# Kernel optimization log

Hardware: AMD Instinct MI355X
Metric: run time of the kernel (lower is better)

The kernel has to match this reference:

```python
import jax, jax.numpy as jnp
import numpy as np

M = 512          # n_clusters
D_PER = 32       # examples per cluster
FEAT = 1024      # embedding dim
ALPHA = 1.0
N_CLASSES = 128
EPS = 1e-8


def setup_inputs() -> dict:
    key = jax.random.key(0)
    k1, k2 = jax.random.split(key)
    N = M * D_PER
    inp = jax.random.normal(k1, (N, FEAT), dtype=jnp.float32)
    # class label per cluster, repeated d times so each contiguous chunk shares a class
    cluster_classes = jax.random.randint(k2, (M,), 0, N_CLASSES, dtype=jnp.int32)
    target = jnp.repeat(cluster_classes, D_PER)
    return {"input": inp, "target": target}


def reference(input, target):
    N, feat = input.shape
    m, d = M, D_PER
    # cluster assignment: sorted arange(m) repeated d times == repeat(arange(m), d)
    clusters = jnp.repeat(jnp.arange(m), d)                      # [N]
    cluster_classes = target[0 : m * d : d]                      # [m]

    # segment mean over contiguous equal-size chunks (== torch.chunk + mean + stack)
    means = input.reshape(m, d, feat).mean(axis=1)               # [m, feat]

    r2 = jnp.sum(input * input, axis=1, keepdims=True)           # [N,1]
    c2 = jnp.sum(means * means, axis=1)                          # [m]
    sample_costs = r2 + c2[None, :] - 2.0 * (input @ means.T)    # [N, m]

    # distance of each example to its own cluster mean
    intra = jnp.take_along_axis(sample_costs, clusters[:, None], axis=1)[:, 0]  # [N]

    variance = jnp.sum(intra) / float(N - 1)
    var_norm = -1.0 / (2.0 * variance ** 2)

    numerator = jnp.exp(var_norm * intra - ALPHA)                # [N]

    diff_class_mask = (target[:, None] != cluster_classes[None, :]).astype(input.dtype)  # [N,m]
    denominator = jnp.sum(diff_class_mask * jnp.exp(var_norm * sample_costs), axis=1)    # [N]

    losses = jax.nn.relu(-jnp.log(numerator / (denominator + EPS) + EPS))
    total_loss = jnp.mean(losses)

    pred = jnp.argmin(sample_costs, axis=1)                      # [N]
    acc = jnp.mean((pred == clusters).astype(jnp.float32))
    return total_loss, losses, pred, acc
```

## Files before the change

kernel.cpp:

```cpp
#include <hip/hip_runtime.h>
#include <math.h>

#define NCLUST 512
#define DPER 32
#define NFEAT 1024
#define NSAMP (NCLUST * DPER)
#define ALPHA_C 1.0f
#define EPS_C 1e-8f
#define MARGIN_C 0.25f

#define GBM 128
#define GBN 128
#define GBK 32
#define NCHUNK 8

typedef __attribute__((ext_vector_type(4))) float f32x4;
typedef __attribute__((ext_vector_type(8))) _Float16 f16x8;

__device__ __forceinline__ unsigned f2h(float f) {
  _Float16 h = (_Float16)f;
  return (unsigned)__builtin_bit_cast(ushort, h);
}

__device__ __forceinline__ void gload16(const ushort* g, ushort* l) {
  __builtin_amdgcn_global_load_lds(
      (const __attribute__((address_space(1))) unsigned int*)g,
      (__attribute__((address_space(3))) unsigned int*)l, 16, 0, 0);
}

__global__ __launch_bounds__(256) void k_pre(const float* __restrict__ inp,
                                             const int* __restrict__ target,
                                             float* __restrict__ means,
                                             ushort* __restrict__ Bf16,
                                             ushort* __restrict__ Af16,
                                             float* __restrict__ c2,
                                             float* __restrict__ r2g,
                                             float* __restrict__ intra,
                                             float* __restrict__ percl,
                                             int* __restrict__ ccls,
                                             int* __restrict__ wcount) {
  const int m = blockIdx.x;
  const int t = threadIdx.x;
  const int w = t >> 6, l = t & 63;
  __shared__ float ldsm[4][NFEAT];
  __shared__ float meanf[NFEAT];
  __shared__ float red4[4];
  __shared__ float redi[4];
  __shared__ float c2sh;

  const float* rowbase = inp + (size_t)m * DPER * NFEAT;
  ushort* arowbase = Af16 + (size_t)m * DPER * NFEAT;

  float4 macc0 = {0,0,0,0}, macc1 = {0,0,0,0}, macc2 = {0,0,0,0}, macc3 = {0,0,0,0};
  float r2keep[8];

  #pragma unroll 2
  for (int rr = 0; rr < 8; ++rr) {
    const int d = w * 8 + rr;
    const float* rp = rowbase + (size_t)d * NFEAT + l * 4;
    const float4 v0 = *(const float4*)(rp);
    const float4 v1 = *(const float4*)(rp + 256);
    const float4 v2 = *(const float4*)(rp + 512);
    const float4 v3 = *(const float4*)(rp + 768);
    ushort* ap = arowbase + (size_t)d * NFEAT + l * 4;
    uint2 h;
    h.x = f2h(v0.x) | (f2h(v0.y) << 16); h.y = f2h(v0.z) | (f2h(v0.w) << 16);
    *(uint2*)(ap) = h;
    h.x = f2h(v1.x) | (f2h(v1.y) << 16); h.y = f2h(v1.z) | (f2h(v1.w) << 16);
    *(uint2*)(ap + 256) = h;
    h.x = f2h(v2.x) | (f2h(v2.y) << 16); h.y = f2h(v2.z) | (f2h(v2.w) << 16);
    *(uint2*)(ap + 512) = h;
    h.x = f2h(v3.x) | (f2h(v3.y) << 16); h.y = f2h(v3.z) | (f2h(v3.w) << 16);
    *(uint2*)(ap + 768) = h;
    macc0.x += v0.x; macc0.y += v0.y; macc0.z += v0.z; macc0.w += v0.w;
    macc1.x += v1.x; macc1.y += v1.y; macc1.z += v1.z; macc1.w += v1.w;
    macc2.x += v2.x; macc2.y += v2.y; macc2.z += v2.z; macc2.w += v2.w;
    macc3.x += v3.x; macc3.y += v3.y; macc3.z += v3.z; macc3.w += v3.w;
    float p = v0.x*v0.x + v0.y*v0.y + v0.z*v0.z + v0.w*v0.w
            + v1.x*v1.x + v1.y*v1.y + v1.z*v1.z + v1.w*v1.w
            + v2.x*v2.x + v2.y*v2.y + v2.z*v2.z + v2.w*v2.w
            + v3.x*v3.x + v3.y*v3.y + v3.z*v3.z + v3.w*v3.w;
    #pragma unroll
    for (int off = 32; off; off >>= 1) p += __shfl_down(p, off);
    r2keep[rr] = p;
  }
  if (l == 0) {
    #pragma unroll
    for (int rr = 0; rr < 8; ++rr) r2g[m * DPER + w * 8 + rr] = r2keep[rr];
  }
  *(float4*)&ldsm[w][0 * 256 + l * 4] = macc0;
  *(float4*)&ldsm[w][1 * 256 + l * 4] = macc1;
  *(float4*)&ldsm[w][2 * 256 + l * 4] = macc2;
  *(float4*)&ldsm[w][3 * 256 + l * 4] = macc3;
  __syncthreads();
  float4 s0 = *(const float4*)&ldsm[0][t * 4];
  float4 s1 = *(const float4*)&ldsm[1][t * 4];
  float4 s2 = *(const float4*)&ldsm[2][t * 4];
  float4 s3 = *(const float4*)&ldsm[3][t * 4];
  const float inv = 1.0f / 32.0f;
  float4 mn;
  mn.x = (s0.x + s1.x + s2.x + s3.x) * inv;
  mn.y = (s0.y + s1.y + s2.y + s3.y) * inv;
  mn.z = (s0.z + s1.z + s2.z + s3.z) * inv;
  mn.w = (s0.w + s1.w + s2.w + s3.w) * inv;
  *(float4*)(means + (size_t)m * NFEAT + t * 4) = mn;
  uint2 bw;
  bw.x = f2h(mn.x) | (f2h(mn.y) << 16);
  bw.y = f2h(mn.z) | (f2h(mn.w) << 16);
  *(uint2*)&Bf16[(size_t)m * NFEAT + t * 4] = bw;
  *(float4*)&meanf[t * 4] = mn;
  float sq = mn.x * mn.x + mn.y * mn.y + mn.z * mn.z + mn.w * mn.w;
  #pragma unroll
  for (int off = 32; off; off >>= 1) sq += __shfl_down(sq, off);
  if (l == 0) red4[w] = sq;
  __syncthreads();
  if (t == 0) {
    const float cc = red4[0] + red4[1] + red4[2] + red4[3];
    c2sh = cc;
    c2[m] = cc;
    ccls[m] = target[m * DPER];
    if (m == 0) *wcount = 0;
  }
  __syncthreads();
  const float c2v = c2sh;
  float sintra = 0.f;
  #pragma unroll 2
  for (int rr = 0; rr < 8; ++rr) {
    const int d = w * 8 + rr;
    const float* rp = rowbase + (size_t)d * NFEAT + l * 4;
    const float4 v0 = *(const float4*)(rp);
    const float4 v1 = *(const float4*)(rp + 256);
    const float4 v2 = *(const float4*)(rp + 512);
    const float4 v3 = *(const float4*)(rp + 768);
    const float4 m0 = *(const float4*)&meanf[0 * 256 + l * 4];
    const float4 m1 = *(const float4*)&meanf[1 * 256 + l * 4];
    const float4 m2 = *(const float4*)&meanf[2 * 256 + l * 4];
    const float4 m3 = *(const float4*)&meanf[3 * 256 + l * 4];
    float p = v0.x*m0.x + v0.y*m0.y + v0.z*m0.z + v0.w*m0.w
            + v1.x*m1.x + v1.y*m1.y + v1.z*m1.z + v1.w*m1.w
            + v2.x*m2.x + v2.y*m2.y + v2.z*m2.z + v2.w*m2.w
            + v3.x*m3.x + v3.y*m3.y + v3.z*m3.z + v3.w*m3.w;
    #pragma unroll
    for (int off = 32; off; off >>= 1) p += __shfl_down(p, off);
    if (l == 0) {
      const float iv = r2keep[rr] + c2v - 2.0f * p;
      intra[m * DPER + d] = iv;
      sintra += iv;
    }
  }
  if (l == 0) redi[w] = sintra;
  __syncthreads();
  if (t == 0) percl[m] = redi[0] + redi[1] + redi[2] + redi[3];
}

__global__ __launch_bounds__(256) void k_var(const float* __restrict__ percl,
                                             float* __restrict__ vn) {
  const int t = threadIdx.x;
  float s = percl[t] + percl[t + 256];
  __shared__ float red[4];
  #pragma unroll
  for (int off = 32; off > 0; off >>= 1) s += __shfl_down(s, off);
  if ((t & 63) == 0) red[t >> 6] = s;
  __syncthreads();
  if (t == 0) {
    float tot = red[0] + red[1] + red[2] + red[3];
    float var = tot / (float)(NSAMP - 1);
    vn[0] = -1.0f / (2.0f * var * var);
  }
}

__global__ __launch_bounds__(256, 3) void k_gemm(
    const ushort* __restrict__ Af16, const ushort* __restrict__ Bf16,
    const float* __restrict__ c2, const float* __restrict__ r2,
    const float* __restrict__ vnp, const int* __restrict__ ccls,
    const int* __restrict__ target,
    float* __restrict__ den_p, float* __restrict__ minv_p,
    float* __restrict__ minv2_p, float* __restrict__ minc_p) {
  __shared__ ushort As[GBM * GBK];
  __shared__ ushort Bs[GBN * GBK];
  const int t = threadIdx.x;
  const int l = t & 63, w = t >> 6;
  const int wg = (blockIdx.x & 7) * 64 + (blockIdx.x >> 3);
  const int rowblk = wg >> 2, colblk = wg & 3;
  const int row0 = rowblk * GBM, c0 = colblk * GBN;
  const int wr = w >> 1, wc = w & 1;

  const int sR = l >> 2;
  const int sg = (l & 3) ^ (sR & 3);
  const ushort* srcA0 = Af16 + (size_t)(row0 + w * 32 + sR) * NFEAT + sg * 8;
  const ushort* srcA1 = srcA0 + 16 * NFEAT;
  const ushort* srcB0 = Bf16 + (size_t)(c0 + w * 32 + sR) * NFEAT + sg * 8;
  const ushort* srcB1 = srcB0 + 16 * NFEAT;
  ushort* ldsA0 = As + w * 32 * GBK;
  ushort* ldsA1 = ldsA0 + 16 * GBK;
  ushort* ldsB0 = Bs + w * 32 * GBK;
  ushort* ldsB1 = ldsB0 + 16 * GBK;

  const int fr = l & 15, fq = l >> 4;
  const int ch = ((fq ^ (fr & 3)) * 8);

  f32x4 acc[4][4];
  #pragma unroll
  for (int i = 0; i < 4; ++i)
    #pragma unroll
    for (int j = 0; j < 4; ++j) acc[i][j] = (f32x4){0.f, 0.f, 0.f, 0.f};

  for (int ks = 0; ks < NFEAT / GBK; ++ks) {
    __syncthreads();
    gload16(srcA0, ldsA0); gload16(srcA1, ldsA1);
    gload16(srcB0, ldsB0); gload16(srcB1, ldsB1);
    srcA0 += GBK; srcA1 += GBK; srcB0 += GBK; srcB1 += GBK;
    __syncthreads();
    f16x8 a[4], b[4];
    #pragma unroll
    for (int i = 0; i < 4; ++i)
      a[i] = *(const f16x8*)&As[(wr * 64 + i * 16 + fr) * GBK + ch];
    #pragma unroll
    for (int j = 0; j < 4; ++j)
      b[j] = *(const f16x8*)&Bs[(wc * 64 + j * 16 + fr) * GBK + ch];
    #pragma unroll
    for (int i = 0; i < 4; ++i)
      #pragma unroll
      for (int j = 0; j < 4; ++j)
        acc[i][j] = __builtin_amdgcn_mfma_f32_16x16x32_f16(a[i], b[j], acc[i][j], 0, 0, 0);
  }

  const float vn = vnp[0];
  float c2j[4]; int clsj[4];
  #pragma unroll
  for (int j = 0; j < 4; ++j) {
    const int c = c0 + wc * 64 + j * 16 + fr;
    c2j[j] = c2[c];
    clsj[j] = ccls[c];
  }
  const int colchunk = colblk * 2 + wc;
  #pragma unroll
  for (int i = 0; i < 4; ++i) {
    const int rbase = row0 + wr * 64 + i * 16 + fq * 4;
    float r2v[4]; int tg[4];
    #pragma unroll
    for (int v = 0; v < 4; ++v) { r2v[v] = r2[rbase + v]; tg[v] = target[rbase + v]; }
    #pragma unroll
    for (int v = 0; v < 4; ++v) {
      float den = 0.f, bv = 3.4e38f, bv2 = 3.4e38f;
      int bc = 1 << 30;
      #pragma unroll
      for (int j = 0; j < 4; ++j) {
        const float cost = r2v[v] + c2j[j] - 2.0f * acc[i][j][v];
        if (clsj[j] != tg[v]) den += __expf(vn * cost);
        if (cost < bv) { bv2 = bv; bv = cost; bc = c0 + wc * 64 + j * 16 + fr; }
        else if (cost < bv2) { bv2 = cost; }
      }
      #pragma unroll
      for (int off = 1; off < 16; off <<= 1) {
        den += __shfl_xor(den, off);
        const float ov = __shfl_xor(bv, off);
        const float ov2 = __shfl_xor(bv2, off);
        const int oc = __shfl_xor(bc, off);
        const float nb2 = fminf(fminf(bv2, ov2), fmaxf(bv, ov));
        if (ov < bv || (ov == bv && oc < bc)) { bv = ov; bc = oc; }
        bv2 = nb2;
      }
      if (fr == 0) {
        const int idx = colchunk * NSAMP + rbase + v;
        den_p[idx] = den;
        minv_p[idx] = bv;
        minv2_p[idx] = bv2;
        minc_p[idx] = (float)bc;
      }
    }
  }
}

__global__ __launch_bounds__(256) void k_fin2(const float* __restrict__ den_p,
                                              const float* __restrict__ minv_p,
                                              const float* __restrict__ minv2_p,
                                              const float* __restrict__ minc_p,
                                              const float* __restrict__ intra,
                                              const float* __restrict__ vnp,
                                              float* __restrict__ losses,
                                              int* __restrict__ wl,
                                              int* __restrict__ wcount,
                                              unsigned long long* __restrict__ slots) {
  const int row = blockIdx.x * 256 + threadIdx.x;
  float den = 0.f, bv = 3.4e38f, bv2 = 3.4e38f, bc = 0.f;
  #pragma unroll
  for (int k = 0; k < NCHUNK; ++k) {
    den += den_p[k * NSAMP + row];
    const float v = minv_p[k * NSAMP + row];
    const float v2 = minv2_p[k * NSAMP + row];
    const float c = minc_p[k * NSAMP + row];
    const float nb2 = fminf(fminf(bv2, v2), fmaxf(bv, v));
    if (v < bv) { bv = v; bc = c; }
    bv2 = nb2;
  }
  const float num = expf(vnp[0] * intra[row] - ALPHA_C);
  const float ratio = num / (den + EPS_C) + EPS_C;
  float loss = -logf(ratio);
  losses[row] = loss > 0.f ? loss : 0.f;
  if (bv2 - bv < MARGIN_C) {
    slots[row] = 0xFFFFFFFFFFFFFFFFULL;
    int i = atomicAdd(wcount, 1);
    wl[i] = row;
  } else {
    slots[row] = ((unsigned long long)__float_as_uint(bv) << 32) | (unsigned)(int)bc;
  }
}

__global__ __launch_bounds__(256) void k_fix(const float* __restrict__ inp,
                                             const float* __restrict__ means,
                                             const float* __restrict__ c2,
                                             const float* __restrict__ r2,
                                             const int* __restrict__ wl,
                                             const int* __restrict__ wcount,
                                             unsigned long long* __restrict__ slots) {
  __shared__ float rbuf[NFEAT];
  const int t = threadIdx.x;
  const int l = t & 63, w = t >> 6;
  const int cnt = *wcount;
  const int chunk = blockIdx.x & 63;
  for (int wi = blockIdx.x >> 6; wi < cnt; wi += gridDim.x >> 6) {
    const int row = wl[wi];
    __syncthreads();
    *(float4*)&rbuf[t * 4] = *(const float4*)(inp + (size_t)row * NFEAT + t * 4);
    __syncthreads();
    float rb[16];
    #pragma unroll
    for (int q = 0; q < 4; ++q) {
      const float4 v = *(const float4*)&rbuf[q * 256 + l * 4];
      rb[q * 4 + 0] = v.x; rb[q * 4 + 1] = v.y;
      rb[q * 4 + 2] = v.z; rb[q * 4 + 3] = v.w;
    }
    const float r2v = r2[row];
    #pragma unroll
    for (int cc = 0; cc < 2; ++cc) {
      const int c = chunk * 8 + w * 2 + cc;
      const float* mp = means + (size_t)c * NFEAT + l * 4;
      float dot = 0.f;
      #pragma unroll
      for (int q = 0; q < 4; ++q) {
        const float4 m4 = *(const float4*)(mp + q * 256);
        dot += m4.x * rb[q * 4 + 0] + m4.y * rb[q * 4 + 1] +
               m4.z * rb[q * 4 + 2] + m4.w * rb[q * 4 + 3];
      }
      #pragma unroll
      for (int off = 32; off; off >>= 1) dot += __shfl_down(dot, off);
      if (l == 0) {
        const float cost = r2v + c2[c] - 2.0f * dot;
        const unsigned long long enc =
            ((unsigned long long)__float_as_uint(cost) << 32) | (unsigned)c;
        atomicMin(&slots[row], enc);
      }
    }
  }
}

__global__ __launch_bounds__(256) void k_final(const float* __restrict__ losses,
                                               const unsigned long long* __restrict__ slots,
                                               float* __restrict__ preds,
                                               float* __restrict__ out) {
  const int t = threadIdx.x;
  float s = 0.f, cnt = 0.f;
  for (int i = t; i < NSAMP; i += 256) {
    s += losses[i];
    const int p = (int)(unsigned)(slots[i] & 0xFFFFFFFFULL);
    preds[i] = (float)p;
    cnt += (p == (i >> 5)) ? 1.f : 0.f;
  }
  __shared__ float redS[4], redC[4];
  #pragma unroll
  for (int off = 32; off > 0; off >>= 1) {
    s += __shfl_down(s, off);
    cnt += __shfl_down(cnt, off);
  }
  if ((t & 63) == 0) { redS[t >> 6] = s; redC[t >> 6] = cnt; }
  __syncthreads();
  if (t == 0) {
    out[0] = (redS[0] + redS[1] + redS[2] + redS[3]) / (float)NSAMP;
    out[1 + 2 * NSAMP] = (redC[0] + redC[1] + redC[2] + redC[3]) / (float)NSAMP;
  }
}

extern "C" void kernel_launch(void* const* d_in, const int* in_sizes, int n_in,
                              void* d_out, int out_size, void* d_ws, size_t ws_size,
                              hipStream_t stream) {
  const float* inp = (const float*)d_in[0];
  const int* target = (const int*)d_in[1];
  float* out = (float*)d_out;

  ushort* Af16 = (ushort*)d_ws;
  ushort* Bf16 = Af16 + (size_t)NSAMP * NFEAT;
  unsigned long long* slots =
      (unsigned long long*)(Bf16 + (size_t)NCLUST * NFEAT);
  float* means = (float*)(slots + NSAMP);
  float* c2 = means + (size_t)NCLUST * NFEAT;
  float* r2 = c2 + NCLUST;
  float* intra = r2 + NSAMP;
  float* vn = intra + NSAMP;
  float* percl = vn + 1;
  int* ccls = (int*)(percl + NCLUST);
  float* den_p = (float*)(ccls + NCLUST);
  float* minv_p = den_p + NCHUNK * NSAMP;
  float* minv2_p = minv_p + NCHUNK * NSAMP;
  float* minc_p = minv2_p + NCHUNK * NSAMP;
  int* wl = (int*)(minc_p + NCHUNK * NSAMP);
  int* wcount = wl + NSAMP;

  float* losses = out + 1;
  float* preds = out + 1 + NSAMP;

  hipLaunchKernelGGL(k_pre, dim3(NCLUST), dim3(256), 0, stream,
                     inp, target, means, Bf16, Af16, c2, r2, intra, percl, ccls, wcount);
  hipLaunchKernelGGL(k_var, dim3(1), dim3(256), 0, stream, percl, vn);
  hipLaunchKernelGGL(k_gemm, dim3(512), dim3(256), 0, stream,
                     Af16, Bf16, c2, r2, vn, ccls, target,
                     den_p, minv_p, minv2_p, minc_p);
  hipLaunchKernelGGL(k_fin2, dim3(NSAMP / 256), dim3(256), 0, stream,
                     den_p, minv_p, minv2_p, minc_p, intra, vn, losses,
                     wl, wcount, slots);
  hipLaunchKernelGGL(k_fix, dim3(2048), dim3(256), 0, stream,
                     inp, means, c2, r2, wl, wcount, slots);
  hipLaunchKernelGGL(k_final, dim3(1), dim3(256), 0, stream,
                     losses, slots, preds, out);
}
```

Measured before the change: 100.7 us.

## Double-buffer GEMM LDS tiles and fold variance reduction into consumers

The GEMM main loop now uses two LDS buffers, issuing the next tile's global-to-LDS loads before computing on the current one, with explicit vmcnt waits and raw barriers. The goal is to overlap memory latency with MFMA work instead of serialising load and compute each step. The separate single-block variance kernel is removed, and each GEMM and finalize block recomputes the variance from the per-cluster sums, which saves one launch at the cost of redundant small reductions. Launch bounds drop from 3 to 2 waves per SIMD because LDS use doubles.

```diff
diff --git a/kernel.cpp b/kernel.cpp
--- a/kernel.cpp
+++ b/kernel.cpp
@@ -153,31 +153,16 @@
   if (t == 0) percl[m] = redi[0] + redi[1] + redi[2] + redi[3];
 }
 
-__global__ __launch_bounds__(256) void k_var(const float* __restrict__ percl,
-                                             float* __restrict__ vn) {
-  const int t = threadIdx.x;
-  float s = percl[t] + percl[t + 256];
-  __shared__ float red[4];
-  #pragma unroll
-  for (int off = 32; off > 0; off >>= 1) s += __shfl_down(s, off);
-  if ((t & 63) == 0) red[t >> 6] = s;
-  __syncthreads();
-  if (t == 0) {
-    float tot = red[0] + red[1] + red[2] + red[3];
-    float var = tot / (float)(NSAMP - 1);
-    vn[0] = -1.0f / (2.0f * var * var);
-  }
-}
-
-__global__ __launch_bounds__(256, 3) void k_gemm(
+__global__ __launch_bounds__(256, 2) void k_gemm(
     const ushort* __restrict__ Af16, const ushort* __restrict__ Bf16,
     const float* __restrict__ c2, const float* __restrict__ r2,
-    const float* __restrict__ vnp, const int* __restrict__ ccls,
+    const float* __restrict__ percl, const int* __restrict__ ccls,
     const int* __restrict__ target,
     float* __restrict__ den_p, float* __restrict__ minv_p,
     float* __restrict__ minv2_p, float* __restrict__ minc_p) {
-  __shared__ ushort As[GBM * GBK];
-  __shared__ ushort Bs[GBN * GBK];
+  __shared__ ushort As[2][GBM * GBK];
+  __shared__ ushort Bs[2][GBN * GBK];
+  __shared__ float redv[4];
   const int t = threadIdx.x;
   const int l = t & 63, w = t >> 6;
   const int wg = (blockIdx.x & 7) * 64 + (blockIdx.x >> 3);
@@ -187,14 +172,10 @@
 
   const int sR = l >> 2;
   const int sg = (l & 3) ^ (sR & 3);
-  const ushort* srcA0 = Af16 + (size_t)(row0 + w * 32 + sR) * NFEAT + sg * 8;
-  const ushort* srcA1 = srcA0 + 16 * NFEAT;
-  const ushort* srcB0 = Bf16 + (size_t)(c0 + w * 32 + sR) * NFEAT + sg * 8;
-  const ushort* srcB1 = srcB0 + 16 * NFEAT;
-  ushort* ldsA0 = As + w * 32 * GBK;
-  ushort* ldsA1 = ldsA0 + 16 * GBK;
-  ushort* ldsB0 = Bs + w * 32 * GBK;
-  ushort* ldsB1 = ldsB0 + 16 * GBK;
+  const ushort* sA0 = Af16 + (size_t)(row0 + w * 32 + sR) * NFEAT + sg * 8;
+  const ushort* sA1 = sA0 + 16 * NFEAT;
+  const ushort* sB0 = Bf16 + (size_t)(c0 + w * 32 + sR) * NFEAT + sg * 8;
+  const ushort* sB1 = sB0 + 16 * NFEAT;
 
   const int fr = l & 15, fq = l >> 4;
   const int ch = ((fq ^ (fr & 3)) * 8);
@@ -205,27 +186,58 @@
     #pragma unroll
     for (int j = 0; j < 4; ++j) acc[i][j] = (f32x4){0.f, 0.f, 0.f, 0.f};
 
-  for (int ks = 0; ks < NFEAT / GBK; ++ks) {
-    __syncthreads();
-    gload16(srcA0, ldsA0); gload16(srcA1, ldsA1);
-    gload16(srcB0, ldsB0); gload16(srcB1, ldsB1);
-    srcA0 += GBK; srcA1 += GBK; srcB0 += GBK; srcB1 += GBK;
-    __syncthreads();
-    f16x8 a[4], b[4];
-    #pragma unroll
-    for (int i = 0; i < 4; ++i)
-      a[i] = *(const f16x8*)&As[(wr * 64 + i * 16 + fr) * GBK + ch];
-    #pragma unroll
-    for (int j = 0; j < 4; ++j)
-      b[j] = *(const f16x8*)&Bs[(wc * 64 + j * 16 + fr) * GBK + ch];
-    #pragma unroll
-    for (int i = 0; i < 4; ++i)
-      #pragma unroll
-      for (int j = 0; j < 4; ++j)
-        acc[i][j] = __builtin_amdgcn_mfma_f32_16x16x32_f16(a[i], b[j], acc[i][j], 0, 0, 0);
-  }
-
-  const float vn = vnp[0];
+#define STAGE(bi, ks) do {                                        \
+    gload16(sA0 + (ks) * GBK, &As[bi][w * 32 * GBK]);             \
+    gload16(sA1 + (ks) * GBK, &As[bi][w * 32 * GBK + 16 * GBK]);  \
+    gload16(sB0 + (ks) * GBK, &Bs[bi][w * 32 * GBK]);             \
+    gload16(sB1 + (ks) * GBK, &Bs[bi][w * 32 * GBK + 16 * GBK]);  \
+  } while (0)
+
+#define COMPUTE(bi) do {                                                     \
+    f16x8 a[4], b[4];                                                        \
+    _Pragma("unroll") for (int i = 0; i < 4; ++i)                            \
+      a[i] = *(const f16x8*)&As[bi][(wr * 64 + i * 16 + fr) * GBK + ch];     \
+    _Pragma("unroll") for (int j = 0; j < 4; ++j)                            \
+      b[j] = *(const f16x8*)&Bs[bi][(wc * 64 + j * 16 + fr) * GBK + ch];     \
+    _Pragma("unroll") for (int i = 0; i < 4; ++i)                            \
+      _Pragma("unroll") for (int j = 0; j < 4; ++j)                          \
+        acc[i][j] = __builtin_amdgcn_mfma_f32_16x16x32_f16(a[i], b[j],       \
+                                                           acc[i][j], 0,0,0);\
+  } while (0)
+
+  STAGE(0, 0);
+  #pragma unroll 1
+  for (int ks = 0; ks < NFEAT / GBK - 2; ks += 2) {
+    STAGE(1, ks + 1);
+    asm volatile("s_waitcnt vmcnt(4)" ::: "memory");
+    __builtin_amdgcn_s_barrier();
+    COMPUTE(0);
+    __builtin_amdgcn_s_barrier();
+    STAGE(0, ks + 2);
+    asm volatile("s_waitcnt vmcnt(4)" ::: "memory");
+    __builtin_amdgcn_s_barrier();
+    COMPUTE(1);
+    __builtin_amdgcn_s_barrier();
+  }
+  STAGE(1, NFEAT / GBK - 1);
+  asm volatile("s_waitcnt vmcnt(4)" ::: "memory");
+  __builtin_amdgcn_s_barrier();
+  COMPUTE(0);
+  __builtin_amdgcn_s_barrier();
+  asm volatile("s_waitcnt vmcnt(0)" ::: "memory");
+  __builtin_amdgcn_s_barrier();
+  COMPUTE(1);
+#undef STAGE
+#undef COMPUTE
+
+  float vs = percl[t] + percl[t + 256];
+  #pragma unroll
+  for (int off = 32; off; off >>= 1) vs += __shfl_down(vs, off);
+  if (l == 0) redv[w] = vs;
+  __syncthreads();
+  const float var = (redv[0] + redv[1] + redv[2] + redv[3]) / (float)(NSAMP - 1);
+  const float vn = -1.0f / (2.0f * var * var);
+
   float c2j[4]; int clsj[4];
   #pragma unroll
   for (int j = 0; j < 4; ++j) {
@@ -277,12 +289,22 @@
                                               const float* __restrict__ minv2_p,
                                               const float* __restrict__ minc_p,
                                               const float* __restrict__ intra,
-                                              const float* __restrict__ vnp,
+                                              const float* __restrict__ percl,
                                               float* __restrict__ losses,
                                               int* __restrict__ wl,
                                               int* __restrict__ wcount,
                                               unsigned long long* __restrict__ slots) {
-  const int row = blockIdx.x * 256 + threadIdx.x;
+  __shared__ float redv[4];
+  const int t = threadIdx.x;
+  float vs = percl[t] + percl[t + 256];
+  #pragma unroll
+  for (int off = 32; off; off >>= 1) vs += __shfl_down(vs, off);
+  if ((t & 63) == 0) redv[t >> 6] = vs;
+  __syncthreads();
+  const float var = (redv[0] + redv[1] + redv[2] + redv[3]) / (float)(NSAMP - 1);
+  const float vn = -1.0f / (2.0f * var * var);
+
+  const int row = blockIdx.x * 256 + t;
   float den = 0.f, bv = 3.4e38f, bv2 = 3.4e38f, bc = 0.f;
   #pragma unroll
   for (int k = 0; k < NCHUNK; ++k) {
@@ -294,7 +316,7 @@
     if (v < bv) { bv = v; bc = c; }
     bv2 = nb2;
   }
-  const float num = expf(vnp[0] * intra[row] - ALPHA_C);
+  const float num = expf(vn * intra[row] - ALPHA_C);
   const float ratio = num / (den + EPS_C) + EPS_C;
   float loss = -logf(ratio);
   losses[row] = loss > 0.f ? loss : 0.f;
@@ -411,12 +433,11 @@
 
   hipLaunchKernelGGL(k_pre, dim3(NCLUST), dim3(256), 0, stream,
                      inp, target, means, Bf16, Af16, c2, r2, intra, percl, ccls, wcount);
-  hipLaunchKernelGGL(k_var, dim3(1), dim3(256), 0, stream, percl, vn);
   hipLaunchKernelGGL(k_gemm, dim3(512), dim3(256), 0, stream,
-                     Af16, Bf16, c2, r2, vn, ccls, target,
+                     Af16, Bf16, c2, r2, percl, ccls, target,
                      den_p, minv_p, minv2_p, minc_p);
   hipLaunchKernelGGL(k_fin2, dim3(NSAMP / 256), dim3(256), 0, stream,
-                     den_p, minv_p, minv2_p, minc_p, intra, vn, losses,
+                     den_p, minv_p, minv2_p, minc_p, intra, percl, losses,
                      wl, wcount, slots);
   hipLaunchKernelGGL(k_fix, dim3(2048), dim3(256), 0, stream,
                      inp, means, c2, r2, wl, wcount, slots);
```

After: 98.09 us. -2.6%, faster.
